# Kernel tuning notes

Measured on AMD Instinct MI355X. Metric: run time of the kernel, lower is better.

## Reference

```python
import jax, jax.numpy as jnp
import numpy as np

N_NODES = 100_000
N_EDGES = 1_600_000
HIDDEN = 64
EPS = 1e-5  # eqx.nn.RMSNorm default eps


def setup_inputs() -> dict:
    key = jax.random.key(0)
    k1, k2, k3 = jax.random.split(key, 3)
    x = jax.random.normal(k1, (N_NODES, HIDDEN), dtype=jnp.float32)
    # edges[0] = target node i, edges[1] = source node j  (a[i, j] = 1 => edge j -> i)
    edges = jax.random.randint(k2, (2, N_EDGES), 0, N_NODES, dtype=jnp.int32)
    W = jax.random.normal(k3, (HIDDEN, HIDDEN), dtype=jnp.float32) * (1.0 / np.sqrt(HIDDEN))
    b = jnp.zeros((HIDDEN,), dtype=jnp.float32)
    norm_weight = jnp.ones((HIDDEN,), dtype=jnp.float32)
    norm_bias = jnp.zeros((HIDDEN,), dtype=jnp.float32)
    return {"x": x, "edges": edges, "W": W, "b": b,
            "norm_weight": norm_weight, "norm_bias": norm_bias}


def reference(x, edges, W, b, norm_weight, norm_bias):
    n_nodes = x.shape[0]
    # vmap(Linear) + relu:  m = relu(x @ W.T + b)
    m = jax.nn.relu(jnp.einsum('nd,kd->nk', x, W) + b)
    # a @ m : sum-aggregate messages from source j into target i
    dst, src = edges[0], edges[1]
    agg = jax.ops.segment_sum(m[src], dst, num_segments=n_nodes)
    # residual + RMSNorm (per-node)
    h = x + agg
    inv_rms = jax.lax.rsqrt(jnp.mean(h * h, axis=-1, keepdims=True) + EPS)
    return norm_weight * (h * inv_rms) + norm_bias
```

## Files before the change

kernel.cpp:

```cpp
#include <hip/hip_runtime.h>
#include <hip/hip_bf16.h>

#define N_NODES 100000
#define N_EDGES 1600000
#define HID 64

#define NG 196
#define GROUPS 511
#define GSTRIDE 512
#define NREP 2
#define RCAP 2048
#define EPT 16
#define BIN_BLOCKS 391
#define LIN_BLOCKS 1563

#define TILES 13
#define TCAP 384
#define GTHREADS 768
#define GWAVES 12

using bf16 = __hip_bfloat16;
typedef __attribute__((ext_vector_type(8))) short short8;
typedef __attribute__((ext_vector_type(4))) short short4v;
typedef __attribute__((ext_vector_type(4))) float float4v;

__device__ __forceinline__ float bfbits2f(unsigned short u) {
    union { unsigned int i; float f; } v;
    v.i = ((unsigned int)u) << 16;
    return v.f;
}
__device__ __forceinline__ unsigned short f2bfbits(float f) {
    union { float f; unsigned int i; } v;
    v.f = f;
    unsigned int r = v.i + 0x7fffu + ((v.i >> 16) & 1u);
    return (unsigned short)(r >> 16);
}

__global__ __launch_bounds__(256) void k_init(
    const float* __restrict__ W, int* __restrict__ gcur,
    unsigned short* __restrict__ Wfhi, unsigned short* __restrict__ Wflo)
{
    const int t = blockIdx.x * 256 + threadIdx.x;
    for (int i = t; i < NREP * GSTRIDE; i += 512) gcur[i] = 0;
    for (int o = t; o < HID * HID; o += 512) {
        const int j = o & 7, l = (o >> 3) & 63, ksnt = o >> 9;
        const int ks = ksnt & 1, nt = ksnt >> 1;
        const int c = l & 15, q = l >> 4;
        const float f = W[(size_t)(nt * 16 + c) * HID + ks * 32 + q * 8 + j];
        const unsigned short h = f2bfbits(f);
        Wfhi[o] = h;
        Wflo[o] = f2bfbits(f - bfbits2f(h));
    }
}

__global__ __launch_bounds__(256, 4) void k_prep2(
    const float* __restrict__ x, const unsigned short* __restrict__ Wfhi,
    const unsigned short* __restrict__ Wflo, const float* __restrict__ b,
    bf16* __restrict__ m,
    const int* __restrict__ edges, int* __restrict__ gcur,
    int* __restrict__ binned)
{
    __shared__ union SM {
        struct { float xs[64 * 65]; } lin;
        struct { int cnt[GSTRIDE]; int base[GSTRIDE]; } bin;
    } sm;
    const int t = threadIdx.x;

    if (blockIdx.x < LIN_BLOCKS) {
        const int nb0 = blockIdx.x * 64;
        const float4* xg = reinterpret_cast<const float4*>(x) + (size_t)nb0 * 16;
        #pragma unroll
        for (int k = 0; k < 4; ++k) {
            const int f4 = t + k * 256;
            float4 v = make_float4(0.f, 0.f, 0.f, 0.f);
            if (nb0 * 16 + f4 < N_NODES * 16) v = xg[f4];
            const int r = f4 >> 4, fc = (f4 & 15) * 4;
            float* dst = &sm.lin.xs[r * 65 + fc];
            dst[0] = v.x; dst[1] = v.y; dst[2] = v.z; dst[3] = v.w;
        }
        __syncthreads();

        const int wv = t >> 6, l = t & 63;
        const int c = l & 15, q = l >> 4;
        const int tile = blockIdx.x * 4 + wv;
        if (tile >= N_NODES / 16) return;
        const int nb = tile * 16;

        const short8* wfh = reinterpret_cast<const short8*>(Wfhi);
        const short8* wfl = reinterpret_cast<const short8*>(Wflo);
        short8 Bhi[4][2], Blo[4][2];
        #pragma unroll
        for (int nt = 0; nt < 4; ++nt)
            #pragma unroll
            for (int ks = 0; ks < 2; ++ks) {
                const int fi = (nt * 2 + ks) * 64 + l;
                Bhi[nt][ks] = wfh[fi];
                Blo[nt][ks] = wfl[fi];
            }

        short8 Ahi[2];
        #pragma unroll
        for (int ks = 0; ks < 2; ++ks) {
            const float* xsrc = &sm.lin.xs[(wv * 16 + c) * 65 + ks * 32 + q * 8];
            #pragma unroll
            for (int j = 0; j < 8; ++j)
                Ahi[ks][j] = (short)f2bfbits(xsrc[j]);
        }

        float4v acc[4];
        #pragma unroll
        for (int nt = 0; nt < 4; ++nt) {
            const float bias = b[nt * 16 + c];
            acc[nt] = (float4v){bias, bias, bias, bias};
            #pragma unroll
            for (int ks = 0; ks < 2; ++ks) {
                acc[nt] = __builtin_amdgcn_mfma_f32_16x16x32_bf16(Ahi[ks], Bhi[nt][ks], acc[nt], 0, 0, 0);
                acc[nt] = __builtin_amdgcn_mfma_f32_16x16x32_bf16(Ahi[ks], Blo[nt][ks], acc[nt], 0, 0, 0);
            }
        }

        unsigned short* mp = reinterpret_cast<unsigned short*>(m);
        #pragma unroll
        for (int nt = 0; nt < 4; ++nt)
            #pragma unroll
            for (int rg = 0; rg < 4; ++rg) {
                const float v = fmaxf(acc[nt][rg], 0.0f);
                mp[(size_t)(nb + q * 4 + rg) * HID + nt * 16 + c] = f2bfbits(v);
            }
    } else {
        int* cnt  = sm.bin.cnt;
        int* base = sm.bin.base;
        const int bb = blockIdx.x - LIN_BLOCKS;
        for (int i = t; i < GSTRIDE; i += 256) cnt[i] = 0;
        __syncthreads();

        const int e0 = bb * (256 * EPT);
        int gk[EPT], pk[EPT], sl[EPT];
        #pragma unroll
        for (int k = 0; k < EPT; ++k) {
            const int e = e0 + k * 256 + t;
            if (e < N_EDGES) {
                const int dst = edges[e];
                const int src = edges[N_EDGES + e];
                const int g = (int)((unsigned)dst / NG);
                gk[k] = g;
                pk[k] = ((dst - g * NG) << 17) | src;
                sl[k] = atomicAdd(&cnt[g], 1);
            } else gk[k] = -1;
        }
        __syncthreads();
        const int r = bb & (NREP - 1);
        for (int i = t; i < GROUPS; i += 256) {
            const int cc = cnt[i];
            base[i] = cc ? atomicAdd(&gcur[r * GSTRIDE + i], cc) : 0;
        }
        __syncthreads();
        #pragma unroll
        for (int k = 0; k < EPT; ++k) {
            if (gk[k] >= 0) {
                const int pos = base[gk[k]] + sl[k];
                if ((unsigned)pos < RCAP)
                    binned[(size_t)(r * GSTRIDE + gk[k]) * RCAP + pos] = pk[k];
            }
        }
    }
}

#define TRREAD(dst, OFF) \
    asm volatile("ds_read_b64_tr_b16 %0, %1 offset:" #OFF \
                 : "=v"(dst) : "v"(traddr) : "memory")

__global__ __launch_bounds__(GTHREADS, 6) void k_gather_mfma(
    const float* __restrict__ x, const bf16* __restrict__ m,
    const int* __restrict__ gcur, const int* __restrict__ binned,
    const float* __restrict__ nw, const float* __restrict__ nbias,
    float* __restrict__ out)
{
    __shared__ int tcnt[TILES];
    __shared__ int tlist[TILES * TCAP];
    __shared__ uint4 stg4[GWAVES * 128];

    const int t = threadIdx.x;
    const int g = blockIdx.x;
    if (t < TILES) tcnt[t] = 0;
    __syncthreads();

    #pragma unroll
    for (int rr = 0; rr < NREP; ++rr) {
        int c = gcur[rr * GSTRIDE + g];
        if (c > RCAP) c = RCAP;
        const int* reg = binned + (size_t)(rr * GSTRIDE + g) * RCAP;
        for (int i = t; i < c; i += GTHREADS) {
            const int pr = reg[i];
            const int tile = pr >> 21;
            const int slot = atomicAdd(&tcnt[tile], 1);
            if (slot < TCAP) tlist[tile * TCAP + slot] = pr & 0x1FFFFF;
        }
    }
    __syncthreads();

    const int wv = t >> 6, l = t & 63;
    const int q = l >> 4;
    const int node16 = l & 15;
    const int fq = l & 7;
    const int sr = l >> 3;
    const int stg_c = ((fq >> 1) << 9) | ((l >> 5) << 7) | ((sr & 3) << 5) | ((l & 1) << 4);
    const int kq0 = ((sr >> 2) << 3) + (sr & 3);
    const int kq1 = (((sr + 8) >> 2) << 3) + (sr & 3);
    char* stg_wave = (char*)(&stg4[0]) + (wv << 11);
    const unsigned traddr = (unsigned)(size_t)stg_wave + (unsigned)(l << 3);
    const uint4* mv = reinterpret_cast<const uint4*>(m);

    for (int tile = wv; tile < TILES; tile += GWAVES) {
        int K = tcnt[tile];
        if (K > TCAP) K = TCAP;
        const int lbase = tile * TCAP;
        float4v acc0 = {0.f, 0.f, 0.f, 0.f};
        float4v acc1 = acc0, acc2 = acc0, acc3 = acc0;
        const int nch = (K + 31) >> 5;

        for (int ch = 0; ch < nch; ++ch) {
            const int k0 = ch << 5;
            const int kA0 = k0 + kq0, kA1 = k0 + kq1;
            const int tA0i = (kA0 < K) ? tlist[lbase + kA0] : 0;
            const int tA1i = (kA1 < K) ? tlist[lbase + kA1] : 0;
            const int tB0i = (kA0 + 4 < K) ? tlist[lbase + kA0 + 4] : 0;
            const int tB1i = (kA1 + 4 < K) ? tlist[lbase + kA1 + 4] : 0;
            const uint4 vA0 = mv[(size_t)(tA0i & 0x1FFFF) * 8 + fq];
            const uint4 vA1 = mv[(size_t)(tA1i & 0x1FFFF) * 8 + fq];
            const uint4 vB0 = mv[(size_t)(tB0i & 0x1FFFF) * 8 + fq];
            const uint4 vB1 = mv[(size_t)(tB1i & 0x1FFFF) * 8 + fq];

            *reinterpret_cast<uint4*>(stg_wave + stg_c) = vA0;
            *reinterpret_cast<uint4*>(stg_wave + stg_c + 256) = vA1;
            short4v tA0, tA1, tA2, tA3;
            TRREAD(tA0, 0); TRREAD(tA1, 512); TRREAD(tA2, 1024); TRREAD(tA3, 1536);

            *reinterpret_cast<uint4*>(stg_wave + stg_c) = vB0;
            *reinterpret_cast<uint4*>(stg_wave + stg_c + 256) = vB1;
            short4v tB0, tB1, tB2, tB3;
            TRREAD(tB0, 0); TRREAD(tB1, 512); TRREAD(tB2, 1024); TRREAD(tB3, 1536);

            const int kb = k0 + (q << 3);
            short8 bh;
            #pragma unroll
            for (int jj = 0; jj < 8; ++jj) {
                const int kk = kb + jj;
                const int tb = (kk < K) ? tlist[lbase + kk] : -1;
                bh[jj] = (short)(((tb >> 17) == node16) ? 0x3F80 : 0);
            }

            asm volatile("s_waitcnt lgkmcnt(0)" ::: "memory");
            __builtin_amdgcn_sched_barrier(0);
            const short8 a0 = __builtin_shufflevector(tA0, tB0, 0, 1, 2, 3, 4, 5, 6, 7);
            const short8 a1 = __builtin_shufflevector(tA1, tB1, 0, 1, 2, 3, 4, 5, 6, 7);
            const short8 a2 = __builtin_shufflevector(tA2, tB2, 0, 1, 2, 3, 4, 5, 6, 7);
            const short8 a3 = __builtin_shufflevector(tA3, tB3, 0, 1, 2, 3, 4, 5, 6, 7);
            acc0 = __builtin_amdgcn_mfma_f32_16x16x32_bf16(a0, bh, acc0, 0, 0, 0);
            acc1 = __builtin_amdgcn_mfma_f32_16x16x32_bf16(a1, bh, acc1, 0, 0, 0);
            acc2 = __builtin_amdgcn_mfma_f32_16x16x32_bf16(a2, bh, acc2, 0, 0, 0);
            acc3 = __builtin_amdgcn_mfma_f32_16x16x32_bf16(a3, bh, acc3, 0, 0, 0);
        }

        const int dl = (tile << 4) + node16;
        const int n = g * NG + dl;
        if (dl < NG && n < N_NODES) {
            const float4* xr = reinterpret_cast<const float4*>(x) + (size_t)n * 16 + q;
            const float4 x0 = xr[0], x1 = xr[4], x2 = xr[8], x3 = xr[12];
            const float h00 = x0.x + acc0[0], h01 = x0.y + acc0[1], h02 = x0.z + acc0[2], h03 = x0.w + acc0[3];
            const float h10 = x1.x + acc1[0], h11 = x1.y + acc1[1], h12 = x1.z + acc1[2], h13 = x1.w + acc1[3];
            const float h20 = x2.x + acc2[0], h21 = x2.y + acc2[1], h22 = x2.z + acc2[2], h23 = x2.w + acc2[3];
            const float h30 = x3.x + acc3[0], h31 = x3.y + acc3[1], h32 = x3.z + acc3[2], h33 = x3.w + acc3[3];
            float ss = h00 * h00 + h01 * h01 + h02 * h02 + h03 * h03
                     + h10 * h10 + h11 * h11 + h12 * h12 + h13 * h13
                     + h20 * h20 + h21 * h21 + h22 * h22 + h23 * h23
                     + h30 * h30 + h31 * h31 + h32 * h32 + h33 * h33;
            ss += __shfl_xor(ss, 16, 64);
            ss += __shfl_xor(ss, 32, 64);
            const float inv = rsqrtf(ss * (1.0f / HID) + 1e-5f);
            const float4* nwp = reinterpret_cast<const float4*>(nw);
            const float4* nbp = reinterpret_cast<const float4*>(nbias);
            float4* op = reinterpret_cast<float4*>(out) + (size_t)n * 16 + q;
            {
                const float4 w = nwp[q], bb = nbp[q];
                float4 o;
                o.x = w.x * h00 * inv + bb.x; o.y = w.y * h01 * inv + bb.y;
                o.z = w.z * h02 * inv + bb.z; o.w = w.w * h03 * inv + bb.w;
                op[0] = o;
            }
            {
                const float4 w = nwp[4 + q], bb = nbp[4 + q];
                float4 o;
                o.x = w.x * h10 * inv + bb.x; o.y = w.y * h11 * inv + bb.y;
                o.z = w.z * h12 * inv + bb.z; o.w = w.w * h13 * inv + bb.w;
                op[4] = o;
            }
            {
                const float4 w = nwp[8 + q], bb = nbp[8 + q];
                float4 o;
                o.x = w.x * h20 * inv + bb.x; o.y = w.y * h21 * inv + bb.y;
                o.z = w.z * h22 * inv + bb.z; o.w = w.w * h23 * inv + bb.w;
                op[8] = o;
            }
            {
                const float4 w = nwp[12 + q], bb = nbp[12 + q];
                float4 o;
                o.x = w.x * h30 * inv + bb.x; o.y = w.y * h31 * inv + bb.y;
                o.z = w.z * h32 * inv + bb.z; o.w = w.w * h33 * inv + bb.w;
                op[12] = o;
            }
        }
    }
}

extern "C" void kernel_launch(void* const* d_in, const int* in_sizes, int n_in,
                              void* d_out, int out_size, void* d_ws, size_t ws_size,
                              hipStream_t stream) {
    const float* x     = (const float*)d_in[0];
    const int*   edges = (const int*)d_in[1];
    const float* W     = (const float*)d_in[2];
    const float* b     = (const float*)d_in[3];
    const float* nw    = (const float*)d_in[4];
    const float* nb    = (const float*)d_in[5];
    float* out = (float*)d_out;

    int* gcur = (int*)d_ws;
    unsigned short* Wfhi = (unsigned short*)((char*)d_ws + (1 << 14));
    unsigned short* Wflo = Wfhi + HID * HID;
    int*  binned = (int*)((char*)d_ws + (1 << 16));
    bf16* m      = (bf16*)((char*)d_ws + (1 << 16) +
                           (size_t)NREP * GSTRIDE * RCAP * sizeof(int));

    k_init<<<2, 256, 0, stream>>>(W, gcur, Wfhi, Wflo);
    k_prep2<<<LIN_BLOCKS + BIN_BLOCKS, 256, 0, stream>>>(x, Wfhi, Wflo, b, m, edges, gcur, binned);
    k_gather_mfma<<<GROUPS, GTHREADS, 0, stream>>>(x, m, gcur, binned, nw, nb, out);
}
```

Baseline: 143.2 us.

## Transpose linear MFMA to load x directly and resize node groups to 192

The linear kernel drops the shared-memory staging of x. It swaps MFMA operands (W as A, x as B), so each lane loads x rows straight from global memory and writes four contiguous bf16 outputs as one ushort4 store. The group size changes from 196 to 192 nodes, which makes it exactly 12 tiles of 16, one per wave. That removes the tile loop and the partial-tile bounds check, and the group count and shared stride grow to match. The intent is to cut LDS traffic, a barrier, scattered 2-byte stores and idle lanes in the aggregation, at the cost of more groups and less coalesced x loads.

```diff
diff --git a/kernel.cpp b/kernel.cpp
--- a/kernel.cpp
+++ b/kernel.cpp
@@ -5,16 +5,16 @@
 #define N_EDGES 1600000
 #define HID 64
 
-#define NG 196
-#define GROUPS 511
-#define GSTRIDE 512
+#define NG 192
+#define GROUPS 521
+#define GSTRIDE 544
 #define NREP 2
 #define RCAP 2048
 #define EPT 16
 #define BIN_BLOCKS 391
 #define LIN_BLOCKS 1563
 
-#define TILES 13
+#define TILES 12
 #define TCAP 384
 #define GTHREADS 768
 #define GWAVES 12
@@ -60,26 +60,10 @@
     const int* __restrict__ edges, int* __restrict__ gcur,
     int* __restrict__ binned)
 {
-    __shared__ union SM {
-        struct { float xs[64 * 65]; } lin;
-        struct { int cnt[GSTRIDE]; int base[GSTRIDE]; } bin;
-    } sm;
+    __shared__ struct { int cnt[GSTRIDE]; int base[GSTRIDE]; } sm;
     const int t = threadIdx.x;
 
     if (blockIdx.x < LIN_BLOCKS) {
-        const int nb0 = blockIdx.x * 64;
-        const float4* xg = reinterpret_cast<const float4*>(x) + (size_t)nb0 * 16;
-        #pragma unroll
-        for (int k = 0; k < 4; ++k) {
-            const int f4 = t + k * 256;
-            float4 v = make_float4(0.f, 0.f, 0.f, 0.f);
-            if (nb0 * 16 + f4 < N_NODES * 16) v = xg[f4];
-            const int r = f4 >> 4, fc = (f4 & 15) * 4;
-            float* dst = &sm.lin.xs[r * 65 + fc];
-            dst[0] = v.x; dst[1] = v.y; dst[2] = v.z; dst[3] = v.w;
-        }
-        __syncthreads();
-
         const int wv = t >> 6, l = t & 63;
         const int c = l & 15, q = l >> 4;
         const int tile = blockIdx.x * 4 + wv;
@@ -88,48 +72,54 @@
 
         const short8* wfh = reinterpret_cast<const short8*>(Wfhi);
         const short8* wfl = reinterpret_cast<const short8*>(Wflo);
-        short8 Bhi[4][2], Blo[4][2];
+        short8 Whi[4][2], Wlo[4][2];
         #pragma unroll
         for (int nt = 0; nt < 4; ++nt)
             #pragma unroll
             for (int ks = 0; ks < 2; ++ks) {
                 const int fi = (nt * 2 + ks) * 64 + l;
-                Bhi[nt][ks] = wfh[fi];
-                Blo[nt][ks] = wfl[fi];
-            }
-
-        short8 Ahi[2];
+                Whi[nt][ks] = wfh[fi];
+                Wlo[nt][ks] = wfl[fi];
+            }
+
+        short8 Xf[2];
+        const float4* xg4 = reinterpret_cast<const float4*>(x) + (size_t)(nb + c) * 16;
         #pragma unroll
         for (int ks = 0; ks < 2; ++ks) {
-            const float* xsrc = &sm.lin.xs[(wv * 16 + c) * 65 + ks * 32 + q * 8];
-            #pragma unroll
-            for (int j = 0; j < 8; ++j)
-                Ahi[ks][j] = (short)f2bfbits(xsrc[j]);
+            const float4 v0 = xg4[ks * 8 + q * 2];
+            const float4 v1 = xg4[ks * 8 + q * 2 + 1];
+            Xf[ks][0] = (short)f2bfbits(v0.x); Xf[ks][1] = (short)f2bfbits(v0.y);
+            Xf[ks][2] = (short)f2bfbits(v0.z); Xf[ks][3] = (short)f2bfbits(v0.w);
+            Xf[ks][4] = (short)f2bfbits(v1.x); Xf[ks][5] = (short)f2bfbits(v1.y);
+            Xf[ks][6] = (short)f2bfbits(v1.z); Xf[ks][7] = (short)f2bfbits(v1.w);
         }
 
         float4v acc[4];
+        const float4* b4 = reinterpret_cast<const float4*>(b);
         #pragma unroll
         for (int nt = 0; nt < 4; ++nt) {
-            const float bias = b[nt * 16 + c];
-            acc[nt] = (float4v){bias, bias, bias, bias};
+            const float4 bq = b4[nt * 4 + q];
+            acc[nt] = (float4v){bq.x, bq.y, bq.z, bq.w};
             #pragma unroll
             for (int ks = 0; ks < 2; ++ks) {
-                acc[nt] = __builtin_amdgcn_mfma_f32_16x16x32_bf16(Ahi[ks], Bhi[nt][ks], acc[nt], 0, 0, 0);
-                acc[nt] = __builtin_amdgcn_mfma_f32_16x16x32_bf16(Ahi[ks], Blo[nt][ks], acc[nt], 0, 0, 0);
-            }
-        }
-
-        unsigned short* mp = reinterpret_cast<unsigned short*>(m);
-        #pragma unroll
-        for (int nt = 0; nt < 4; ++nt)
-            #pragma unroll
-            for (int rg = 0; rg < 4; ++rg) {
-                const float v = fmaxf(acc[nt][rg], 0.0f);
-                mp[(size_t)(nb + q * 4 + rg) * HID + nt * 16 + c] = f2bfbits(v);
-            }
+                acc[nt] = __builtin_amdgcn_mfma_f32_16x16x32_bf16(Whi[nt][ks], Xf[ks], acc[nt], 0, 0, 0);
+                acc[nt] = __builtin_amdgcn_mfma_f32_16x16x32_bf16(Wlo[nt][ks], Xf[ks], acc[nt], 0, 0, 0);
+            }
+        }
+
+        ushort4* mp4 = reinterpret_cast<ushort4*>(m);
+        #pragma unroll
+        for (int nt = 0; nt < 4; ++nt) {
+            ushort4 u;
+            u.x = f2bfbits(fmaxf(acc[nt][0], 0.0f));
+            u.y = f2bfbits(fmaxf(acc[nt][1], 0.0f));
+            u.z = f2bfbits(fmaxf(acc[nt][2], 0.0f));
+            u.w = f2bfbits(fmaxf(acc[nt][3], 0.0f));
+            mp4[(size_t)(nb + c) * 16 + nt * 4 + q] = u;
+        }
     } else {
-        int* cnt  = sm.bin.cnt;
-        int* base = sm.bin.base;
+        int* cnt  = sm.cnt;
+        int* base = sm.base;
         const int bb = blockIdx.x - LIN_BLOCKS;
         for (int i = t; i < GSTRIDE; i += 256) cnt[i] = 0;
         __syncthreads();
@@ -211,7 +201,8 @@
     const unsigned traddr = (unsigned)(size_t)stg_wave + (unsigned)(l << 3);
     const uint4* mv = reinterpret_cast<const uint4*>(m);
 
-    for (int tile = wv; tile < TILES; tile += GWAVES) {
+    const int tile = wv;
+    {
         int K = tcnt[tile];
         if (K > TCAP) K = TCAP;
         const int lbase = tile * TCAP;
@@ -264,7 +255,7 @@
 
         const int dl = (tile << 4) + node16;
         const int n = g * NG + dl;
-        if (dl < NG && n < N_NODES) {
+        if (n < N_NODES) {
             const float4* xr = reinterpret_cast<const float4*>(x) + (size_t)n * 16 + q;
             const float4 x0 = xr[0], x1 = xr[4], x2 = xr[8], x3 = xr[12];
             const float h00 = x0.x + acc0[0], h01 = x0.y + acc0[1], h02 = x0.z + acc0[2], h03 = x0.w + acc0[3];
```

After: 155.9 us. +8.9%, slower.

## Software-pipeline gathered message loads and give each wave exactly one tile

Applied to the files above, without the earlier changes.

Each group now covers 192 nodes in 12 tiles, so each of the 12 waves owns exactly one tile. The per-element bound checks go away because tile lists are padded to whole chunks with a tag that matches no node. The gather of message rows is double-buffered: the next chunk's list indices and m-rows are loaded while the current chunk is staged through LDS and fed to the MFMAs. The B-matrix index reads use vectorized int4 loads with a permuted k ordering that matches the new staging layout. This trades extra registers for in-flight loads and more groups in exchange for hiding gather latency and removing the idle 13th tile.

```diff
diff --git a/kernel.cpp b/kernel.cpp
--- a/kernel.cpp
+++ b/kernel.cpp
@@ -5,19 +5,20 @@
 #define N_EDGES 1600000
 #define HID 64
 
-#define NG 196
-#define GROUPS 511
-#define GSTRIDE 512
+#define NG 192
+#define GROUPS 521
+#define GSTRIDE 544
 #define NREP 2
 #define RCAP 2048
 #define EPT 16
 #define BIN_BLOCKS 391
 #define LIN_BLOCKS 1563
 
-#define TILES 13
+#define TILES 12
 #define TCAP 384
 #define GTHREADS 768
 #define GWAVES 12
+#define PADTAG (16 << 17)
 
 using bf16 = __hip_bfloat16;
 typedef __attribute__((ext_vector_type(8))) short short8;
@@ -202,53 +203,67 @@
     const int wv = t >> 6, l = t & 63;
     const int q = l >> 4;
     const int node16 = l & 15;
-    const int fq = l & 7;
-    const int sr = l >> 3;
-    const int stg_c = ((fq >> 1) << 9) | ((l >> 5) << 7) | ((sr & 3) << 5) | ((l & 1) << 4);
-    const int kq0 = ((sr >> 2) << 3) + (sr & 3);
-    const int kq1 = (((sr + 8) >> 2) << 3) + (sr & 3);
+    const int h  = l & 1;
+    const int r2 = (l >> 1) & 3;
+    const int ft = (l >> 3) & 3;
+    const int qb = (l >> 5) & 1;
+    const int fq = ft * 2 + h;
+    const int sA0 = qb * 8 + r2 * 2;
+    const int wbyte = ft * 512 + qb * 128 + r2 * 32 + h * 16;
     char* stg_wave = (char*)(&stg4[0]) + (wv << 11);
     const unsigned traddr = (unsigned)(size_t)stg_wave + (unsigned)(l << 3);
     const uint4* mv = reinterpret_cast<const uint4*>(m);
 
-    for (int tile = wv; tile < TILES; tile += GWAVES) {
-        int K = tcnt[tile];
-        if (K > TCAP) K = TCAP;
-        const int lbase = tile * TCAP;
-        float4v acc0 = {0.f, 0.f, 0.f, 0.f};
-        float4v acc1 = acc0, acc2 = acc0, acc3 = acc0;
-        const int nch = (K + 31) >> 5;
+    const int tile = wv;
+    int K = tcnt[tile];
+    if (K > TCAP) K = TCAP;
+    const int lbase = tile * TCAP;
+    const int nch = (K + 31) >> 5;
+
+    for (int i = K + l; i < nch * 32; i += 64) tlist[lbase + i] = PADTAG;
+
+    float4v acc0 = {0.f, 0.f, 0.f, 0.f};
+    float4v acc1 = acc0, acc2 = acc0, acc3 = acc0;
+
+    if (nch > 0) {
+        int2 pa = *reinterpret_cast<const int2*>(&tlist[lbase + sA0]);
+        int2 pb = *reinterpret_cast<const int2*>(&tlist[lbase + sA0 + 16]);
+        uint4 dA0 = mv[(size_t)(pa.x & 0x1FFFF) * 8 + fq];
+        uint4 dA1 = mv[(size_t)(pb.x & 0x1FFFF) * 8 + fq];
+        uint4 dB0 = mv[(size_t)(pa.y & 0x1FFFF) * 8 + fq];
+        uint4 dB1 = mv[(size_t)(pb.y & 0x1FFFF) * 8 + fq];
 
         for (int ch = 0; ch < nch; ++ch) {
             const int k0 = ch << 5;
-            const int kA0 = k0 + kq0, kA1 = k0 + kq1;
-            const int tA0i = (kA0 < K) ? tlist[lbase + kA0] : 0;
-            const int tA1i = (kA1 < K) ? tlist[lbase + kA1] : 0;
-            const int tB0i = (kA0 + 4 < K) ? tlist[lbase + kA0 + 4] : 0;
-            const int tB1i = (kA1 + 4 < K) ? tlist[lbase + kA1 + 4] : 0;
-            const uint4 vA0 = mv[(size_t)(tA0i & 0x1FFFF) * 8 + fq];
-            const uint4 vA1 = mv[(size_t)(tA1i & 0x1FFFF) * 8 + fq];
-            const uint4 vB0 = mv[(size_t)(tB0i & 0x1FFFF) * 8 + fq];
-            const uint4 vB1 = mv[(size_t)(tB1i & 0x1FFFF) * 8 + fq];
-
-            *reinterpret_cast<uint4*>(stg_wave + stg_c) = vA0;
-            *reinterpret_cast<uint4*>(stg_wave + stg_c + 256) = vA1;
+            const int kn = (ch + 1 < nch) ? (k0 + 32) : 0;
+            const int2 npa = *reinterpret_cast<const int2*>(&tlist[lbase + kn + sA0]);
+            const int2 npb = *reinterpret_cast<const int2*>(&tlist[lbase + kn + sA0 + 16]);
+            const uint4 nA0 = mv[(size_t)(npa.x & 0x1FFFF) * 8 + fq];
+            const uint4 nA1 = mv[(size_t)(npb.x & 0x1FFFF) * 8 + fq];
+            const uint4 nB0 = mv[(size_t)(npa.y & 0x1FFFF) * 8 + fq];
+            const uint4 nB1 = mv[(size_t)(npb.y & 0x1FFFF) * 8 + fq];
+
+            const int4 t0 = *reinterpret_cast<const int4*>(&tlist[lbase + k0 + q * 8]);
+            const int4 t1 = *reinterpret_cast<const int4*>(&tlist[lbase + k0 + q * 8 + 4]);
+            short8 bh;
+            bh[0] = (short)(((t0.x >> 17) == node16) ? 0x3F80 : 0);
+            bh[4] = (short)(((t0.y >> 17) == node16) ? 0x3F80 : 0);
+            bh[1] = (short)(((t0.z >> 17) == node16) ? 0x3F80 : 0);
+            bh[5] = (short)(((t0.w >> 17) == node16) ? 0x3F80 : 0);
+            bh[2] = (short)(((t1.x >> 17) == node16) ? 0x3F80 : 0);
+            bh[6] = (short)(((t1.y >> 17) == node16) ? 0x3F80 : 0);
+            bh[3] = (short)(((t1.z >> 17) == node16) ? 0x3F80 : 0);
+            bh[7] = (short)(((t1.w >> 17) == node16) ? 0x3F80 : 0);
+
+            *reinterpret_cast<uint4*>(stg_wave + wbyte) = dA0;
+            *reinterpret_cast<uint4*>(stg_wave + wbyte + 256) = dA1;
             short4v tA0, tA1, tA2, tA3;
             TRREAD(tA0, 0); TRREAD(tA1, 512); TRREAD(tA2, 1024); TRREAD(tA3, 1536);
 
-            *reinterpret_cast<uint4*>(stg_wave + stg_c) = vB0;
-            *reinterpret_cast<uint4*>(stg_wave + stg_c + 256) = vB1;
+            *reinterpret_cast<uint4*>(stg_wave + wbyte) = dB0;
+            *reinterpret_cast<uint4*>(stg_wave + wbyte + 256) = dB1;
             short4v tB0, tB1, tB2, tB3;
             TRREAD(tB0, 0); TRREAD(tB1, 512); TRREAD(tB2, 1024); TRREAD(tB3, 1536);
-
-            const int kb = k0 + (q << 3);
-            short8 bh;
-            #pragma unroll
-            for (int jj = 0; jj < 8; ++jj) {
-                const int kk = kb + jj;
-                const int tb = (kk < K) ? tlist[lbase + kk] : -1;
-                bh[jj] = (short)(((tb >> 17) == node16) ? 0x3F80 : 0);
-            }
 
             asm volatile("s_waitcnt lgkmcnt(0)" ::: "memory");
             __builtin_amdgcn_sched_barrier(0);
@@ -260,55 +275,58 @@
             acc1 = __builtin_amdgcn_mfma_f32_16x16x32_bf16(a1, bh, acc1, 0, 0, 0);
             acc2 = __builtin_amdgcn_mfma_f32_16x16x32_bf16(a2, bh, acc2, 0, 0, 0);
             acc3 = __builtin_amdgcn_mfma_f32_16x16x32_bf16(a3, bh, acc3, 0, 0, 0);
-        }
-
-        const int dl = (tile << 4) + node16;
-        const int n = g * NG + dl;
-        if (dl < NG && n < N_NODES) {
-            const float4* xr = reinterpret_cast<const float4*>(x) + (size_t)n * 16 + q;
-            const float4 x0 = xr[0], x1 = xr[4], x2 = xr[8], x3 = xr[12];
-            const float h00 = x0.x + acc0[0], h01 = x0.y + acc0[1], h02 = x0.z + acc0[2], h03 = x0.w + acc0[3];
-            const float h10 = x1.x + acc1[0], h11 = x1.y + acc1[1], h12 = x1.z + acc1[2], h13 = x1.w + acc1[3];
-            const float h20 = x2.x + acc2[0], h21 = x2.y + acc2[1], h22 = x2.z + acc2[2], h23 = x2.w + acc2[3];
-            const float h30 = x3.x + acc3[0], h31 = x3.y + acc3[1], h32 = x3.z + acc3[2], h33 = x3.w + acc3[3];
-            float ss = h00 * h00 + h01 * h01 + h02 * h02 + h03 * h03
-                     + h10 * h10 + h11 * h11 + h12 * h12 + h13 * h13
-                     + h20 * h20 + h21 * h21 + h22 * h22 + h23 * h23
-                     + h30 * h30 + h31 * h31 + h32 * h32 + h33 * h33;
-            ss += __shfl_xor(ss, 16, 64);
-            ss += __shfl_xor(ss, 32, 64);
-            const float inv = rsqrtf(ss * (1.0f / HID) + 1e-5f);
-            const float4* nwp = reinterpret_cast<const float4*>(nw);
-            const float4* nbp = reinterpret_cast<const float4*>(nbias);
-            float4* op = reinterpret_cast<float4*>(out) + (size_t)n * 16 + q;
-            {
-                const float4 w = nwp[q], bb = nbp[q];
-                float4 o;
-                o.x = w.x * h00 * inv + bb.x; o.y = w.y * h01 * inv + bb.y;
-                o.z = w.z * h02 * inv + bb.z; o.w = w.w * h03 * inv + bb.w;
-                op[0] = o;
-            }
-            {
-                const float4 w = nwp[4 + q], bb = nbp[4 + q];
-                float4 o;
-                o.x = w.x * h10 * inv + bb.x; o.y = w.y * h11 * inv + bb.y;
-                o.z = w.z * h12 * inv + bb.z; o.w = w.w * h13 * inv + bb.w;
-                op[4] = o;
-            }
-            {
-                const float4 w = nwp[8 + q], bb = nbp[8 + q];
-                float4 o;
-                o.x = w.x * h20 * inv + bb.x; o.y = w.y * h21 * inv + bb.y;
-                o.z = w.z * h22 * inv + bb.z; o.w = w.w * h23 * inv + bb.w;
-                op[8] = o;
-            }
-            {
-                const float4 w = nwp[12 + q], bb = nbp[12 + q];
-                float4 o;
-                o.x = w.x * h30 * inv + bb.x; o.y = w.y * h31 * inv + bb.y;
-                o.z = w.z * h32 * inv + bb.z; o.w = w.w * h33 * inv + bb.w;
-                op[12] = o;
-            }
+
+            pa = npa; pb = npb;
+            dA0 = nA0; dA1 = nA1; dB0 = nB0; dB1 = nB1;
+        }
+    }
+
+    const int dl = (tile << 4) + node16;
+    const int n = g * NG + dl;
+    if (n < N_NODES) {
+        const float4* xr = reinterpret_cast<const float4*>(x) + (size_t)n * 16 + q;
+        const float4 x0 = xr[0], x1 = xr[4], x2 = xr[8], x3 = xr[12];
+        const float h00 = x0.x + acc0[0], h01 = x0.y + acc0[1], h02 = x0.z + acc0[2], h03 = x0.w + acc0[3];
+        const float h10 = x1.x + acc1[0], h11 = x1.y + acc1[1], h12 = x1.z + acc1[2], h13 = x1.w + acc1[3];
+        const float h20 = x2.x + acc2[0], h21 = x2.y + acc2[1], h22 = x2.z + acc2[2], h23 = x2.w + acc2[3];
+        const float h30 = x3.x + acc3[0], h31 = x3.y + acc3[1], h32 = x3.z + acc3[2], h33 = x3.w + acc3[3];
+        float ss = h00 * h00 + h01 * h01 + h02 * h02 + h03 * h03
+                 + h10 * h10 + h11 * h11 + h12 * h12 + h13 * h13
+                 + h20 * h20 + h21 * h21 + h22 * h22 + h23 * h23
+                 + h30 * h30 + h31 * h31 + h32 * h32 + h33 * h33;
+        ss += __shfl_xor(ss, 16, 64);
+        ss += __shfl_xor(ss, 32, 64);
+        const float inv = rsqrtf(ss * (1.0f / HID) + 1e-5f);
+        const float4* nwp = reinterpret_cast<const float4*>(nw);
+        const float4* nbp = reinterpret_cast<const float4*>(nbias);
+        float4* op = reinterpret_cast<float4*>(out) + (size_t)n * 16 + q;
+        {
+            const float4 w = nwp[q], bb = nbp[q];
+            float4 o;
+            o.x = w.x * h00 * inv + bb.x; o.y = w.y * h01 * inv + bb.y;
+            o.z = w.z * h02 * inv + bb.z; o.w = w.w * h03 * inv + bb.w;
+            op[0] = o;
+        }
+        {
+            const float4 w = nwp[4 + q], bb = nbp[4 + q];
+            float4 o;
+            o.x = w.x * h10 * inv + bb.x; o.y = w.y * h11 * inv + bb.y;
+            o.z = w.z * h12 * inv + bb.z; o.w = w.w * h13 * inv + bb.w;
+            op[4] = o;
+        }
+        {
+            const float4 w = nwp[8 + q], bb = nbp[8 + q];
+            float4 o;
+            o.x = w.x * h20 * inv + bb.x; o.y = w.y * h21 * inv + bb.y;
+            o.z = w.z * h22 * inv + bb.z; o.w = w.w * h23 * inv + bb.w;
+            op[8] = o;
+        }
+        {
+            const float4 w = nwp[12 + q], bb = nbp[12 + q];
+            float4 o;
+            o.x = w.x * h30 * inv + bb.x; o.y = w.y * h31 * inv + bb.y;
+            o.z = w.z * h32 * inv + bb.z; o.w = w.w * h33 * inv + bb.w;
+            op[12] = o;
         }
     }
 }
```

Measured after the change: 150.6 us. 1.05x slower.
